# Kernel tuning notes

Hardware: AMD Instinct MI355X
Metric: run time of the kernel (lower is better)

Reference implementation:

```python
import jax, jax.numpy as jnp
import numpy as np

C = 512
IC = C // 2
BN_EPS = 1e-5

def conv1x1(x, w, b):
    # x: (b,c,h,w), w: (o,c), b: (o,)
    return jnp.einsum('bchw,oc->bohw', x, w) + b[None, :, None, None]

def setup_inputs() -> dict:
    key = jax.random.key(0)
    ks = jax.random.split(key, 9)
    b, h, w = 8, 48, 48
    x = jax.random.normal(ks[0], (b, C, h, w), dtype=jnp.float32)
    s = 1.0 / np.sqrt(C)
    g_w = jax.random.normal(ks[1], (IC, C), dtype=jnp.float32) * s
    g_b = jnp.zeros((IC,), jnp.float32)
    theta_w = jax.random.normal(ks[2], (IC, C), dtype=jnp.float32) * s
    theta_b = jnp.zeros((IC,), jnp.float32)
    phi_w = jax.random.normal(ks[3], (IC, C), dtype=jnp.float32) * s
    phi_b = jnp.zeros((IC,), jnp.float32)
    w_w = jax.random.normal(ks[4], (C, IC), dtype=jnp.float32) * (1.0 / np.sqrt(IC))
    w_b = jnp.zeros((C,), jnp.float32)
    # BatchNorm affine params: initialized to 0 per nn.init.constant_ in source
    bn_gamma = jnp.zeros((C,), jnp.float32)
    bn_beta = jnp.zeros((C,), jnp.float32)
    return {"x": x, "g_w": g_w, "g_b": g_b, "theta_w": theta_w, "theta_b": theta_b,
            "phi_w": phi_w, "phi_b": phi_b, "w_w": w_w, "w_b": w_b,
            "bn_gamma": bn_gamma, "bn_beta": bn_beta}

def reference(x, g_w, g_b, theta_w, theta_b, phi_w, phi_b, w_w, w_b, bn_gamma, bn_beta):
    b, c, h, w = x.shape
    hw = h * w
    g_x = conv1x1(x, g_w, g_b).reshape(b, IC, hw).transpose(0, 2, 1)      # (b,hw,ic)
    theta_x = conv1x1(x, theta_w, theta_b).reshape(b, IC, hw).transpose(0, 2, 1)  # (b,hw,ic)
    phi_x = conv1x1(x, phi_w, phi_b).reshape(b, IC, hw)                    # (b,ic,hw)
    f = jnp.einsum('bqc,bck->bqk', theta_x, phi_x)                         # (b,hw,hw), unscaled
    f_div_C = jax.nn.softmax(f, axis=-1)
    y = jnp.einsum('bqk,bkc->bqc', f_div_C, g_x)                           # (b,hw,ic)
    y = y.transpose(0, 2, 1).reshape(b, IC, h, w)
    wy = conv1x1(y, w_w, w_b)                                              # (b,c,h,w)
    # BatchNorm2d in training mode: batch statistics over (b,h,w)
    mean = jnp.mean(wy, axis=(0, 2, 3), keepdims=True)
    var = jnp.var(wy, axis=(0, 2, 3), keepdims=True)
    wy_bn = (wy - mean) / jnp.sqrt(var + BN_EPS)
    wy_bn = wy_bn * bn_gamma[None, :, None, None] + bn_beta[None, :, None, None]
    return wy_bn + x
```

## Files before the change

kernel.cpp:

```cpp
#include <hip/hip_runtime.h>
#include <hip/hip_bf16.h>
#include <stdint.h>

constexpr int Bn  = 8;
constexpr int Cc  = 512;
constexpr int ICc = 256;
constexpr int HWc = 48 * 48;
constexpr float BN_EPS = 1e-5f;

typedef unsigned short u16;
typedef __attribute__((ext_vector_type(8))) short short8;
typedef __attribute__((ext_vector_type(4))) float f32x4;

__device__ __forceinline__ u16 f2bf(float f) {
    uint32_t u = __builtin_bit_cast(uint32_t, f);
    u += 0x7fffu + ((u >> 16) & 1u);
    return (u16)(u >> 16);
}
__device__ __forceinline__ float bf2f(u16 h) {
    uint32_t u = ((uint32_t)h) << 16;
    return __builtin_bit_cast(float, u);
}
__device__ __forceinline__ void load_lds16(const void* g, void* l) {
    __builtin_amdgcn_global_load_lds(
        (const __attribute__((address_space(1))) void*)(uintptr_t)g,
        (__attribute__((address_space(3))) void*)(uintptr_t)l, 16, 0, 0);
}
template <int N> __device__ __forceinline__ void wait_vmcnt() {
    if constexpr (N == 0)      asm volatile("s_waitcnt vmcnt(0)" ::: "memory");
    else if constexpr (N == 3) asm volatile("s_waitcnt vmcnt(3)" ::: "memory");
    else if constexpr (N == 4) asm volatile("s_waitcnt vmcnt(4)" ::: "memory");
    else if constexpr (N == 6) asm volatile("s_waitcnt vmcnt(6)" ::: "memory");
    else if constexpr (N == 8) asm volatile("s_waitcnt vmcnt(8)" ::: "memory");
}
__device__ __forceinline__ void wait_lgkm0() {
    asm volatile("s_waitcnt lgkmcnt(0)" ::: "memory");
}
__device__ __forceinline__ void barrier_fenced() {
    __builtin_amdgcn_s_barrier();
    asm volatile("" ::: "memory");
}

__global__ __launch_bounds__(256)
void cast_front(const float* __restrict__ th_w, const float* __restrict__ ph_w,
                const float* __restrict__ g_w, const float* __restrict__ th_b,
                const float* __restrict__ ph_b, u16* __restrict__ wcat,
                float* __restrict__ bias_thph) {
    int idx = blockIdx.x * 256 + threadIdx.x;
    if (idx < 98304) {
        const float4* src;
        if (idx < 32768)       src = (const float4*)th_w + idx;
        else if (idx < 65536)  src = (const float4*)ph_w + (idx - 32768);
        else                   src = (const float4*)g_w  + (idx - 65536);
        float4 v = *src;
        ushort4 o;
        o.x = f2bf(v.x); o.y = f2bf(v.y); o.z = f2bf(v.z); o.w = f2bf(v.w);
        ((ushort4*)wcat)[idx] = o;
    } else if (idx < 98816) {
        int i = idx - 98304;
        bias_thph[i] = (i < 256) ? th_b[i] : ph_b[i - 256];
    }
}

__global__ __launch_bounds__(256)
void cast_w(const float* __restrict__ a, u16* __restrict__ out) {
    int idx = blockIdx.x * 256 + threadIdx.x;
    float4 v = ((const float4*)a)[idx];
    ushort4 o;
    o.x = f2bf(v.x); o.y = f2bf(v.y); o.z = f2bf(v.z); o.w = f2bf(v.w);
    ((ushort4*)out)[idx] = o;
}

__global__ __launch_bounds__(256)
void transpose_cast_x(const float* __restrict__ x, u16* __restrict__ xt) {
    __shared__ float t[64][33];
    const int b = blockIdx.z;
    const int p0 = blockIdx.x * 32;
    const int c0 = blockIdx.y * 64;
    const int tx = threadIdx.x & 31, ty = threadIdx.x >> 5;
    const float* xb = x + (size_t)b * Cc * HWc;
#pragma unroll
    for (int r = 0; r < 8; ++r)
        t[r * 8 + ty][tx] = xb[(size_t)(c0 + r * 8 + ty) * HWc + p0 + tx];
    __syncthreads();
    u16* xtb = xt + (size_t)b * HWc * Cc;
    const int cc = (threadIdx.x & 31) * 2, pp = threadIdx.x >> 5;
#pragma unroll
    for (int r = 0; r < 4; ++r) {
        int p = r * 8 + pp;
        ushort2 v;
        v.x = f2bf(t[cc][p]);
        v.y = f2bf(t[cc + 1][p]);
        *(ushort2*)&xtb[(size_t)(p0 + p) * Cc + c0 + cc] = v;
    }
}

template <int TM, int STORE, bool STATS>
__global__ __launch_bounds__(256, 2)
void mfma_gemm(const u16* __restrict__ A, const u16* __restrict__ B,
               void* __restrict__ Cout, const float* __restrict__ bias,
               int bias_mode, int K, int ldA, int ldB, int ldC,
               size_t sA, size_t sB, size_t sC,
               float* __restrict__ s0g, float* __restrict__ s1g) {
    constexpr int MI  = TM / 32;
    constexpr int LPS = (TM == 128) ? 4 : 3;
    __shared__ __align__(16) u16 As[3][TM * 32];
    __shared__ __align__(16) u16 Bs[3][128 * 32];
    const int bz = blockIdx.z;
    const int m0 = blockIdx.y * TM, n0 = blockIdx.x * 128;
    const u16* Ab = A + (size_t)bz * sA + (size_t)m0 * ldA;
    const u16* Bb = B + (size_t)bz * sB + (size_t)n0 * ldB;
    const int tid = threadIdx.x, lane = tid & 63, w = tid >> 6;
    const int wm = (w & 1) * (TM / 2);
    const int wn = (w >> 1) * 64;
    const int quad = lane >> 4, m16 = lane & 15;

    f32x4 acc[MI][4];
#pragma unroll
    for (int i = 0; i < MI; ++i)
#pragma unroll
        for (int j = 0; j < 4; ++j) acc[i][j] = (f32x4){0.f, 0.f, 0.f, 0.f};

    const int L0 = 2 * w * 64 + lane, L1 = L0 + 64;
    const int br0 = L0 >> 2, bc0 = ((L0 & 3) ^ ((L0 >> 3) & 3)) * 8;
    const int br1 = L1 >> 2, bc1 = ((L1 & 3) ^ ((L1 >> 3) & 3)) * 8;
    const int ar0 = (TM == 128) ? br0 : (tid >> 2);
    const int ac0 = (TM == 128) ? bc0 : (((tid & 3) ^ ((tid >> 3) & 3)) * 8);

    auto stage = [&](int buf, int k0) {
        if (TM == 128) {
            load_lds16(Ab + (size_t)ar0 * ldA + k0 + ac0, &As[buf][2 * w * 512]);
            load_lds16(Ab + (size_t)br1 * ldA + k0 + bc1, &As[buf][(2 * w + 1) * 512]);
        } else {
            load_lds16(Ab + (size_t)ar0 * ldA + k0 + ac0, &As[buf][w * 512]);
        }
        load_lds16(Bb + (size_t)br0 * ldB + k0 + bc0, &Bs[buf][2 * w * 512]);
        load_lds16(Bb + (size_t)br1 * ldB + k0 + bc1, &Bs[buf][(2 * w + 1) * 512]);
    };

    const int sq = (quad ^ ((m16 >> 1) & 3)) * 8;

    auto compute = [&](int buf) {
        short8 af[MI], bfv[4];
#pragma unroll
        for (int i = 0; i < MI; ++i)
            af[i] = *(const short8*)&As[buf][(wm + i * 16 + m16) * 32 + sq];
#pragma unroll
        for (int j = 0; j < 4; ++j)
            bfv[j] = *(const short8*)&Bs[buf][(wn + j * 16 + m16) * 32 + sq];
#pragma unroll
        for (int i = 0; i < MI; ++i)
#pragma unroll
            for (int j = 0; j < 4; ++j)
                acc[i][j] = __builtin_amdgcn_mfma_f32_16x16x32_bf16(
                    af[i], bfv[j], acc[i][j], 0, 0, 0);
    };

    const int nt = K / 32;
    stage(0, 0);
    stage(1, 32);

    int cur = 0;
    for (int t = 0; t < nt - 2; ++t) {
        int nxt = cur + 2; if (nxt >= 3) nxt -= 3;
        stage(nxt, (t + 2) * 32);
        wait_vmcnt<2 * LPS>();
        barrier_fenced();
        compute(cur);
        wait_lgkm0();
        barrier_fenced();
        ++cur; if (cur == 3) cur = 0;
    }
    wait_vmcnt<LPS>();
    barrier_fenced();
    compute(cur);
    wait_lgkm0();
    barrier_fenced();
    ++cur; if (cur == 3) cur = 0;
    wait_vmcnt<0>();
    barrier_fenced();
    compute(cur);

    if (bias_mode) {
#pragma unroll
        for (int i = 0; i < MI; ++i)
#pragma unroll
            for (int j = 0; j < 4; ++j)
#pragma unroll
                for (int r = 0; r < 4; ++r)
                    acc[i][j][r] += (bias_mode == 2)
                        ? bias[m0 + wm + i * 16 + quad * 4 + r]
                        : bias[n0 + wn + j * 16 + m16];
    }

    if (STORE == 0) {
        u16* C = (u16*)Cout + (size_t)bz * sC;
#pragma unroll
        for (int i = 0; i < MI; ++i) {
            int m = m0 + wm + i * 16 + quad * 4;
#pragma unroll
            for (int j = 0; j < 4; ++j) {
                int n = n0 + wn + j * 16 + m16;
#pragma unroll
                for (int r = 0; r < 4; ++r)
                    C[(size_t)(m + r) * ldC + n] = f2bf(acc[i][j][r]);
            }
        }
    } else {
        float* C = (float*)Cout + (size_t)bz * sC;
#pragma unroll
        for (int i = 0; i < MI; ++i) {
            int m = m0 + wm + i * 16 + quad * 4;
#pragma unroll
            for (int j = 0; j < 4; ++j) {
                int n = n0 + wn + j * 16 + m16;
#pragma unroll
                for (int r = 0; r < 4; ++r)
                    C[(size_t)(m + r) * ldC + n] = acc[i][j][r];
            }
        }
    }

    if (STATS) {
#pragma unroll
        for (int i = 0; i < MI; ++i) {
#pragma unroll
            for (int r = 0; r < 4; ++r) {
                float v0 = 0.f, v1 = 0.f;
#pragma unroll
                for (int j = 0; j < 4; ++j) {
                    float v = acc[i][j][r];
                    v0 += v;
                    v1 = fmaf(v, v, v1);
                }
#pragma unroll
                for (int off = 8; off; off >>= 1) {
                    v0 += __shfl_down(v0, off, 16);
                    v1 += __shfl_down(v1, off, 16);
                }
                if (m16 == 0) {
                    int m = m0 + wm + i * 16 + quad * 4 + r;
                    atomicAdd(&s0g[m], v0);
                    atomicAdd(&s1g[m], v1);
                }
            }
        }
    }
}

__global__ __launch_bounds__(192)
void softmax_rows(u16* __restrict__ S) {
    const int b = blockIdx.x & 7;
    const int q = blockIdx.x >> 3;
    u16* row = S + ((size_t)b * HWc + q) * (size_t)HWc;
    const int tid = threadIdx.x;

    float v[12];
#pragma unroll
    for (int c = 0; c < 3; ++c) {
        uint2 raw = *(const uint2*)&row[(c * 192 + tid) * 4];
        v[c * 4 + 0] = bf2f((u16)(raw.x & 0xffff));
        v[c * 4 + 1] = bf2f((u16)(raw.x >> 16));
        v[c * 4 + 2] = bf2f((u16)(raw.y & 0xffff));
        v[c * 4 + 3] = bf2f((u16)(raw.y >> 16));
    }
    float m = v[0];
#pragma unroll
    for (int i = 1; i < 12; ++i) m = fmaxf(m, v[i]);
#pragma unroll
    for (int off = 32; off; off >>= 1) m = fmaxf(m, __shfl_down(m, off, 64));
    __shared__ float redm[3], reds[3];
    if ((tid & 63) == 0) redm[tid >> 6] = m;
    __syncthreads();
    m = fmaxf(fmaxf(redm[0], redm[1]), redm[2]);

    float s = 0.f;
#pragma unroll
    for (int i = 0; i < 12; ++i) { v[i] = __expf(v[i] - m); s += v[i]; }
#pragma unroll
    for (int off = 32; off; off >>= 1) s += __shfl_down(s, off, 64);
    if ((tid & 63) == 0) reds[tid >> 6] = s;
    __syncthreads();
    const float rinv = 1.0f / (reds[0] + reds[1] + reds[2]);

#pragma unroll
    for (int c = 0; c < 3; ++c) {
        uint2 o;
        o.x = (uint32_t)f2bf(v[c * 4 + 0] * rinv) |
              ((uint32_t)f2bf(v[c * 4 + 1] * rinv) << 16);
        o.y = (uint32_t)f2bf(v[c * 4 + 2] * rinv) |
              ((uint32_t)f2bf(v[c * 4 + 3] * rinv) << 16);
        *(uint2*)&row[(c * 192 + tid) * 4] = o;
    }
}

__global__ __launch_bounds__(256)
void bn_apply(const float* __restrict__ wy, const float* __restrict__ x,
              const float* __restrict__ s0, const float* __restrict__ s1,
              const float* __restrict__ gamma, const float* __restrict__ beta,
              float* __restrict__ out) {
    const size_t i4 = (size_t)blockIdx.x * 256 + threadIdx.x;
    const size_t base = i4 * 4;
    const int o = (int)((base / HWc) % Cc);
    const float N = (float)(Bn * HWc);
    const float mean = s0[o] / N;
    const float var  = s1[o] / N - mean * mean;
    const float rstd = rsqrtf(var + BN_EPS);
    const float ga = gamma[o];
    const float be = beta[o];
    const float4 w4 = ((const float4*)wy)[i4];
    const float4 x4 = ((const float4*)x)[i4];
    float4 r;
    r.x = (w4.x - mean) * rstd * ga + be + x4.x;
    r.y = (w4.y - mean) * rstd * ga + be + x4.y;
    r.z = (w4.z - mean) * rstd * ga + be + x4.z;
    r.w = (w4.w - mean) * rstd * ga + be + x4.w;
    ((float4*)out)[i4] = r;
}

extern "C" void kernel_launch(void* const* d_in, const int* in_sizes, int n_in,
                              void* d_out, int out_size, void* d_ws, size_t ws_size,
                              hipStream_t stream) {
    const float* x     = (const float*)d_in[0];
    const float* g_w   = (const float*)d_in[1];
    const float* g_b   = (const float*)d_in[2];
    const float* th_w  = (const float*)d_in[3];
    const float* th_b  = (const float*)d_in[4];
    const float* ph_w  = (const float*)d_in[5];
    const float* ph_b  = (const float*)d_in[6];
    const float* w_w   = (const float*)d_in[7];
    const float* w_b   = (const float*)d_in[8];
    const float* gamma = (const float*)d_in[9];
    const float* beta  = (const float*)d_in[10];

    char* base = (char*)d_ws;
    const size_t SZT = (size_t)Bn * HWc * ICc * 2;
    u16* thph = (u16*)base;
    u16* g    = (u16*)(base + 2 * SZT);
    char* Sreg = base + 3 * SZT;
    u16* S    = (u16*)Sreg;
    u16* xt   = (u16*)Sreg;
    u16* wcat = (u16*)(Sreg + (size_t)Bn * HWc * Cc * 2);
    float* bias_thph = (float*)(Sreg + (size_t)Bn * HWc * Cc * 2 + 786432);
    u16* y    = (u16*)base;
    u16* wbf2 = (u16*)(base + SZT);
    float* stats = (float*)(base + SZT + 262144);
    float* wy = (float*)Sreg;

    dim3 blk(256);
    const u16* thphw = wcat;
    const u16* gwb   = wcat + 262144;

    cast_front<<<dim3(386), blk, 0, stream>>>(th_w, ph_w, g_w, th_b, ph_b,
                                              wcat, bias_thph);
    transpose_cast_x<<<dim3(HWc / 32, Cc / 64, Bn), blk, 0, stream>>>(x, xt);

    mfma_gemm<128, 0, false><<<dim3(4, 18, Bn), blk, 0, stream>>>(
        xt, thphw, thph, bias_thph, 1, Cc, Cc, Cc, 512,
        (size_t)HWc * Cc, 0, (size_t)HWc * 512, nullptr, nullptr);

    mfma_gemm<64, 0, false><<<dim3(18, 4, Bn), blk, 0, stream>>>(
        gwb, xt, g, g_b, 2, Cc, Cc, Cc, HWc,
        0, (size_t)HWc * Cc, (size_t)ICc * HWc, nullptr, nullptr);

    mfma_gemm<128, 0, false><<<dim3(18, 18, Bn), blk, 0, stream>>>(
        thph, thph + 256, S, nullptr, 0, ICc, 512, 512, HWc,
        (size_t)HWc * 512, (size_t)HWc * 512, (size_t)HWc * HWc,
        nullptr, nullptr);

    cast_w<<<dim3(128), blk, 0, stream>>>(w_w, wbf2);
    hipMemsetAsync(stats, 0, 2 * Cc * sizeof(float), stream);

    softmax_rows<<<dim3(Bn * HWc), dim3(192), 0, stream>>>(S);

    mfma_gemm<64, 0, false><<<dim3(2, 36, Bn), blk, 0, stream>>>(
        S, g, y, nullptr, 0, HWc, HWc, HWc, ICc,
        (size_t)HWc * HWc, (size_t)ICc * HWc, (size_t)HWc * ICc,
        nullptr, nullptr);

    mfma_gemm<128, 1, true><<<dim3(18, 4, Bn), blk, 0, stream>>>(
        wbf2, y, wy, w_b, 2, ICc, ICc, ICc, HWc,
        0, (size_t)HWc * ICc, (size_t)Cc * HWc, stats, stats + Cc);

    bn_apply<<<dim3((Bn * Cc * HWc) / 4 / 256), blk, 0, stream>>>(
        wy, x, stats, stats + Cc, gamma, beta, (float*)d_out);
}
```

Baseline: 321.1 us.

## Fuse QK^T, softmax and PV into a single flash-attention kernel

Replaces the separate S=QK^T GEMM, row softmax and PV GEMM with one online-softmax kernel that keeps 64-key tiles of scores in LDS and accumulates the output with running max/sum rescaling. This removes the write and re-read of the full bf16 score matrix (8×2304×2304) and two kernel launches, and the workspace layout is rearranged accordingly. In exchange only 288 blocks are launched, V is read straight from global memory without LDS staging, and there are several barriers per tile, which may limit occupancy and latency hiding.

```diff
diff --git a/kernel.cpp b/kernel.cpp
--- a/kernel.cpp
+++ b/kernel.cpp
@@ -248,49 +248,187 @@
     }
 }
 
-__global__ __launch_bounds__(192)
-void softmax_rows(u16* __restrict__ S) {
-    const int b = blockIdx.x & 7;
-    const int q = blockIdx.x >> 3;
-    u16* row = S + ((size_t)b * HWc + q) * (size_t)HWc;
-    const int tid = threadIdx.x;
-
-    float v[12];
-#pragma unroll
-    for (int c = 0; c < 3; ++c) {
-        uint2 raw = *(const uint2*)&row[(c * 192 + tid) * 4];
-        v[c * 4 + 0] = bf2f((u16)(raw.x & 0xffff));
-        v[c * 4 + 1] = bf2f((u16)(raw.x >> 16));
-        v[c * 4 + 2] = bf2f((u16)(raw.y & 0xffff));
-        v[c * 4 + 3] = bf2f((u16)(raw.y >> 16));
-    }
-    float m = v[0];
-#pragma unroll
-    for (int i = 1; i < 12; ++i) m = fmaxf(m, v[i]);
-#pragma unroll
-    for (int off = 32; off; off >>= 1) m = fmaxf(m, __shfl_down(m, off, 64));
-    __shared__ float redm[3], reds[3];
-    if ((tid & 63) == 0) redm[tid >> 6] = m;
+__global__ __launch_bounds__(256, 2)
+void fused_attn(const u16* __restrict__ thph, const u16* __restrict__ gmat,
+                u16* __restrict__ y) {
+    __shared__ __align__(16) u16 Ks[2][64 * 256];
+    __shared__ __align__(16) u16 Sl[64 * 68];
+    __shared__ float alpha_lds[64];
+
+    const int id = blockIdx.x;
+    const int b = id & 7, qi = id >> 3;
+    const int q0 = qi * 64;
+    const u16* tB = thph + (size_t)b * HWc * 512;
+    const u16* gB = gmat + (size_t)b * ICc * HWc;
+    const int tid = threadIdx.x, lane = tid & 63, w = tid >> 6;
+    const int quad = lane >> 4, m16 = lane & 15;
+    const int wq = (w & 1) * 32, wk = (w >> 1) * 32;
+    const int wv = w * 64;
+
+    short8 qf[2][8];
+#pragma unroll
+    for (int i = 0; i < 2; ++i)
+#pragma unroll
+        for (int ds = 0; ds < 8; ++ds)
+            qf[i][ds] = *(const short8*)&tB[(size_t)(q0 + wq + i * 16 + m16) * 512
+                                            + ds * 32 + quad * 8];
+
+    auto stageK = [&](int buf, int k0) {
+#pragma unroll
+        for (int u = 0; u < 8; ++u) {
+            int s = (w * 8 + u) * 64 + lane;
+            int r = s >> 5;
+            int c = s & 31;
+            int sc = c ^ (r & 7);
+            load_lds16(tB + (size_t)(k0 + r) * 512 + 256 + sc * 8,
+                       &Ks[buf][(w * 8 + u) * 512]);
+        }
+    };
+
+    const int sr = w * 16 + (lane >> 2);
+    const int scol = (lane & 3) * 16;
+    float mrow = -3.0e38f, lrow = 0.f;
+
+    f32x4 acc2[4][4];
+#pragma unroll
+    for (int i = 0; i < 4; ++i)
+#pragma unroll
+        for (int j = 0; j < 4; ++j) acc2[i][j] = (f32x4){0.f, 0.f, 0.f, 0.f};
+
+    stageK(0, 0);
+
+    for (int t = 0; t < 36; ++t) {
+        const int buf = t & 1;
+        if (t + 1 < 36) {
+            stageK(buf ^ 1, (t + 1) * 64);
+            wait_vmcnt<8>();
+        } else {
+            wait_vmcnt<0>();
+        }
+        barrier_fenced();
+
+        f32x4 acc1[2][2];
+#pragma unroll
+        for (int i = 0; i < 2; ++i)
+#pragma unroll
+            for (int j = 0; j < 2; ++j) acc1[i][j] = (f32x4){0.f, 0.f, 0.f, 0.f};
+        const u16* kb = &Ks[buf][0];
+#pragma unroll
+        for (int ds = 0; ds < 8; ++ds) {
+            short8 kf[2];
+#pragma unroll
+            for (int j = 0; j < 2; ++j) {
+                int kr = wk + j * 16 + m16;
+                int c  = (ds * 4 + quad) ^ (m16 & 7);
+                kf[j] = *(const short8*)&kb[kr * 256 + c * 8];
+            }
+#pragma unroll
+            for (int i = 0; i < 2; ++i)
+#pragma unroll
+                for (int j = 0; j < 2; ++j)
+                    acc1[i][j] = __builtin_amdgcn_mfma_f32_16x16x32_bf16(
+                        qf[i][ds], kf[j], acc1[i][j], 0, 0, 0);
+        }
+
+#pragma unroll
+        for (int i = 0; i < 2; ++i)
+#pragma unroll
+            for (int j = 0; j < 2; ++j)
+#pragma unroll
+                for (int r = 0; r < 4; ++r)
+                    Sl[(wq + i * 16 + quad * 4 + r) * 68 + wk + j * 16 + m16] =
+                        f2bf(acc1[i][j][r]);
+        wait_lgkm0();
+        barrier_fenced();
+
+        {
+            u16* srow = &Sl[sr * 68 + scol];
+            float v[16];
+            short4 r0 = *(const short4*)&srow[0];
+            short4 r1 = *(const short4*)&srow[4];
+            short4 r2 = *(const short4*)&srow[8];
+            short4 r3 = *(const short4*)&srow[12];
+            v[0]=bf2f((u16)r0.x); v[1]=bf2f((u16)r0.y); v[2]=bf2f((u16)r0.z); v[3]=bf2f((u16)r0.w);
+            v[4]=bf2f((u16)r1.x); v[5]=bf2f((u16)r1.y); v[6]=bf2f((u16)r1.z); v[7]=bf2f((u16)r1.w);
+            v[8]=bf2f((u16)r2.x); v[9]=bf2f((u16)r2.y); v[10]=bf2f((u16)r2.z); v[11]=bf2f((u16)r2.w);
+            v[12]=bf2f((u16)r3.x); v[13]=bf2f((u16)r3.y); v[14]=bf2f((u16)r3.z); v[15]=bf2f((u16)r3.w);
+            float tm = v[0];
+#pragma unroll
+            for (int k = 1; k < 16; ++k) tm = fmaxf(tm, v[k]);
+            tm = fmaxf(tm, __shfl_xor(tm, 1, 64));
+            tm = fmaxf(tm, __shfl_xor(tm, 2, 64));
+            float mn = fmaxf(mrow, tm);
+            float a  = __expf(mrow - mn);
+            float rs = 0.f;
+#pragma unroll
+            for (int k = 0; k < 16; ++k) { v[k] = __expf(v[k] - mn); rs += v[k]; }
+            rs += __shfl_xor(rs, 1, 64);
+            rs += __shfl_xor(rs, 2, 64);
+            lrow = lrow * a + rs;
+            mrow = mn;
+            ushort4 o0 = {f2bf(v[0]), f2bf(v[1]), f2bf(v[2]), f2bf(v[3])};
+            ushort4 o1 = {f2bf(v[4]), f2bf(v[5]), f2bf(v[6]), f2bf(v[7])};
+            ushort4 o2 = {f2bf(v[8]), f2bf(v[9]), f2bf(v[10]), f2bf(v[11])};
+            ushort4 o3 = {f2bf(v[12]), f2bf(v[13]), f2bf(v[14]), f2bf(v[15])};
+            *(ushort4*)&srow[0]  = o0;
+            *(ushort4*)&srow[4]  = o1;
+            *(ushort4*)&srow[8]  = o2;
+            *(ushort4*)&srow[12] = o3;
+            if ((lane & 3) == 0) alpha_lds[sr] = a;
+        }
+        wait_lgkm0();
+        barrier_fenced();
+
+        f32x4 al[4];
+#pragma unroll
+        for (int i = 0; i < 4; ++i)
+            al[i] = *(const f32x4*)&alpha_lds[i * 16 + quad * 4];
+#pragma unroll
+        for (int i = 0; i < 4; ++i)
+#pragma unroll
+            for (int j2 = 0; j2 < 4; ++j2)
+#pragma unroll
+                for (int r = 0; r < 4; ++r) acc2[i][j2][r] *= al[i][r];
+
+        const int kbase = t * 64;
+#pragma unroll
+        for (int ks = 0; ks < 2; ++ks) {
+            short8 pa[4];
+#pragma unroll
+            for (int i = 0; i < 4; ++i) {
+                const u16* pr = &Sl[(i * 16 + m16) * 68 + ks * 32 + quad * 8];
+                short4 lo = *(const short4*)&pr[0];
+                short4 hi = *(const short4*)&pr[4];
+                pa[i] = (short8){lo.x, lo.y, lo.z, lo.w, hi.x, hi.y, hi.z, hi.w};
+            }
+            short8 vb[4];
+#pragma unroll
+            for (int j2 = 0; j2 < 4; ++j2)
+                vb[j2] = *(const short8*)&gB[(size_t)(wv + j2 * 16 + m16) * HWc
+                                             + kbase + ks * 32 + quad * 8];
+#pragma unroll
+            for (int i = 0; i < 4; ++i)
+#pragma unroll
+                for (int j2 = 0; j2 < 4; ++j2)
+                    acc2[i][j2] = __builtin_amdgcn_mfma_f32_16x16x32_bf16(
+                        pa[i], vb[j2], acc2[i][j2], 0, 0, 0);
+        }
+    }
+
     __syncthreads();
-    m = fmaxf(fmaxf(redm[0], redm[1]), redm[2]);
-
-    float s = 0.f;
-#pragma unroll
-    for (int i = 0; i < 12; ++i) { v[i] = __expf(v[i] - m); s += v[i]; }
-#pragma unroll
-    for (int off = 32; off; off >>= 1) s += __shfl_down(s, off, 64);
-    if ((tid & 63) == 0) reds[tid >> 6] = s;
+    if ((lane & 3) == 0) alpha_lds[sr] = 1.0f / lrow;
     __syncthreads();
-    const float rinv = 1.0f / (reds[0] + reds[1] + reds[2]);
-
-#pragma unroll
-    for (int c = 0; c < 3; ++c) {
-        uint2 o;
-        o.x = (uint32_t)f2bf(v[c * 4 + 0] * rinv) |
-              ((uint32_t)f2bf(v[c * 4 + 1] * rinv) << 16);
-        o.y = (uint32_t)f2bf(v[c * 4 + 2] * rinv) |
-              ((uint32_t)f2bf(v[c * 4 + 3] * rinv) << 16);
-        *(uint2*)&row[(c * 192 + tid) * 4] = o;
+
+    u16* yB = y + (size_t)b * HWc * ICc;
+#pragma unroll
+    for (int i = 0; i < 4; ++i) {
+        f32x4 li = *(const f32x4*)&alpha_lds[i * 16 + quad * 4];
+#pragma unroll
+        for (int j2 = 0; j2 < 4; ++j2)
+#pragma unroll
+            for (int r = 0; r < 4; ++r)
+                yB[(size_t)(q0 + i * 16 + quad * 4 + r) * ICc + wv + j2 * 16 + m16] =
+                    f2bf(acc2[i][j2][r] * li[r]);
     }
 }
 
@@ -338,14 +476,13 @@
     u16* thph = (u16*)base;
     u16* g    = (u16*)(base + 2 * SZT);
     char* Sreg = base + 3 * SZT;
-    u16* S    = (u16*)Sreg;
     u16* xt   = (u16*)Sreg;
     u16* wcat = (u16*)(Sreg + (size_t)Bn * HWc * Cc * 2);
     float* bias_thph = (float*)(Sreg + (size_t)Bn * HWc * Cc * 2 + 786432);
-    u16* y    = (u16*)base;
-    u16* wbf2 = (u16*)(base + SZT);
-    float* stats = (float*)(base + SZT + 262144);
-    float* wy = (float*)Sreg;
+    u16* y    = (u16*)Sreg;
+    float* wy = (float*)(Sreg + SZT);
+    u16* wbf2 = (u16*)(Sreg + SZT + (size_t)Bn * Cc * HWc * 4);
+    float* stats = (float*)(Sreg + SZT + (size_t)Bn * Cc * HWc * 4 + 262144);
 
     dim3 blk(256);
     const u16* thphw = wcat;
@@ -363,20 +500,10 @@
         gwb, xt, g, g_b, 2, Cc, Cc, Cc, HWc,
         0, (size_t)HWc * Cc, (size_t)ICc * HWc, nullptr, nullptr);
 
-    mfma_gemm<128, 0, false><<<dim3(18, 18, Bn), blk, 0, stream>>>(
-        thph, thph + 256, S, nullptr, 0, ICc, 512, 512, HWc,
-        (size_t)HWc * 512, (size_t)HWc * 512, (size_t)HWc * HWc,
-        nullptr, nullptr);
-
     cast_w<<<dim3(128), blk, 0, stream>>>(w_w, wbf2);
     hipMemsetAsync(stats, 0, 2 * Cc * sizeof(float), stream);
 
-    softmax_rows<<<dim3(Bn * HWc), dim3(192), 0, stream>>>(S);
-
-    mfma_gemm<64, 0, false><<<dim3(2, 36, Bn), blk, 0, stream>>>(
-        S, g, y, nullptr, 0, HWc, HWc, HWc, ICc,
-        (size_t)HWc * HWc, (size_t)ICc * HWc, (size_t)HWc * ICc,
-        nullptr, nullptr);
+    fused_attn<<<dim3(288), blk, 0, stream>>>(thph, g, y);
 
     mfma_gemm<128, 1, true><<<dim3(18, 4, Bn), blk, 0, stream>>>(
         wbf2, y, wy, w_b, 2, ICc, ICc, ICc, HWc,
```

Result: no change. 323.1 us (+0.6%).

## Fuse QK^T, softmax and PV into a flash-attention style kernel

Applied to the files above, without the earlier changes.

Replaces the separate score GEMM, row softmax and probability-times-V GEMM with one fused kernel that uses online softmax over key tiles of 32, so the full HW×HW score matrix is never written to or read from global memory. K and V tiles are double-buffered in LDS through direct global-to-LDS loads, and both products use 32x32x16 bf16 MFMA. Workspace offsets are rearranged because the S buffer is gone. The cost is a small grid of 576 blocks of 128 threads and heavy per-block register use, which may limit occupancy.

```diff
diff --git a/kernel.cpp b/kernel.cpp
--- a/kernel.cpp
+++ b/kernel.cpp
@@ -11,6 +11,8 @@
 typedef unsigned short u16;
 typedef __attribute__((ext_vector_type(8))) short short8;
 typedef __attribute__((ext_vector_type(4))) float f32x4;
+typedef __attribute__((ext_vector_type(16))) float f32x16;
+typedef __attribute__((ext_vector_type(4))) unsigned int u32x4;
 
 __device__ __forceinline__ u16 f2bf(float f) {
     uint32_t u = __builtin_bit_cast(uint32_t, f);
@@ -248,50 +250,130 @@
     }
 }
 
-__global__ __launch_bounds__(192)
-void softmax_rows(u16* __restrict__ S) {
-    const int b = blockIdx.x & 7;
-    const int q = blockIdx.x >> 3;
-    u16* row = S + ((size_t)b * HWc + q) * (size_t)HWc;
-    const int tid = threadIdx.x;
-
-    float v[12];
-#pragma unroll
-    for (int c = 0; c < 3; ++c) {
-        uint2 raw = *(const uint2*)&row[(c * 192 + tid) * 4];
-        v[c * 4 + 0] = bf2f((u16)(raw.x & 0xffff));
-        v[c * 4 + 1] = bf2f((u16)(raw.x >> 16));
-        v[c * 4 + 2] = bf2f((u16)(raw.y & 0xffff));
-        v[c * 4 + 3] = bf2f((u16)(raw.y >> 16));
-    }
-    float m = v[0];
-#pragma unroll
-    for (int i = 1; i < 12; ++i) m = fmaxf(m, v[i]);
-#pragma unroll
-    for (int off = 32; off; off >>= 1) m = fmaxf(m, __shfl_down(m, off, 64));
-    __shared__ float redm[3], reds[3];
-    if ((tid & 63) == 0) redm[tid >> 6] = m;
-    __syncthreads();
-    m = fmaxf(fmaxf(redm[0], redm[1]), redm[2]);
-
-    float s = 0.f;
-#pragma unroll
-    for (int i = 0; i < 12; ++i) { v[i] = __expf(v[i] - m); s += v[i]; }
-#pragma unroll
-    for (int off = 32; off; off >>= 1) s += __shfl_down(s, off, 64);
-    if ((tid & 63) == 0) reds[tid >> 6] = s;
-    __syncthreads();
-    const float rinv = 1.0f / (reds[0] + reds[1] + reds[2]);
-
-#pragma unroll
-    for (int c = 0; c < 3; ++c) {
-        uint2 o;
-        o.x = (uint32_t)f2bf(v[c * 4 + 0] * rinv) |
-              ((uint32_t)f2bf(v[c * 4 + 1] * rinv) << 16);
-        o.y = (uint32_t)f2bf(v[c * 4 + 2] * rinv) |
-              ((uint32_t)f2bf(v[c * 4 + 3] * rinv) << 16);
-        *(uint2*)&row[(c * 192 + tid) * 4] = o;
-    }
+__global__ __launch_bounds__(128, 2)
+void fused_attn(const u16* __restrict__ thph, const u16* __restrict__ gmat,
+                u16* __restrict__ y) {
+    __shared__ __align__(16) u16 Ks[2][8192];
+    __shared__ __align__(16) u16 Vs[2][8192];
+    const int id = blockIdx.x;
+    const int b = id & 7, qt = id >> 3;
+    const int q0 = qt * 32;
+    const u16* tB = thph + (size_t)b * HWc * 512;
+    const u16* gB = gmat + (size_t)b * ICc * HWc;
+    const int tid = threadIdx.x, lane = tid & 63, w = tid >> 6;
+    const int l31 = lane & 31, h = lane >> 5;
+
+    short8 qf[16];
+#pragma unroll
+    for (int ds = 0; ds < 16; ++ds)
+        qf[ds] = *(const short8*)&tB[(size_t)(q0 + l31) * 512 + ds * 16 + h * 8];
+
+    auto stage = [&](int buf, int t) {
+        const int k0 = t * 32;
+#pragma unroll
+        for (int u = 0; u < 8; ++u) {
+            const int su = w * 8 + u;
+            load_lds16(tB + (size_t)(k0 + l31) * 512 + 256 + (su * 2 + h) * 8,
+                       &Ks[buf][su * 512]);
+        }
+#pragma unroll
+        for (int u = 0; u < 8; ++u) {
+            const int su = w * 8 + u;
+            load_lds16(gB + (size_t)((su & 3) * 64 + lane) * HWc + k0 + (su >> 2) * 8,
+                       &Vs[buf][su * 512]);
+        }
+    };
+
+    float mrow = -3.0e38f, lrow = 0.f;
+    f32x16 acc2[4];
+#pragma unroll
+    for (int vt = 0; vt < 4; ++vt)
+#pragma unroll
+        for (int e = 0; e < 16; ++e) acc2[vt][e] = 0.f;
+
+    stage(0, 0);
+    wait_vmcnt<0>();
+    barrier_fenced();
+
+    constexpr int NT = 72;
+    for (int t = 0; t < NT; ++t) {
+        const int buf = t & 1;
+        if (t + 1 < NT) stage(buf ^ 1, t + 1);
+
+        f32x16 acc1;
+#pragma unroll
+        for (int e = 0; e < 16; ++e) acc1[e] = 0.f;
+#pragma unroll
+        for (int ds = 0; ds < 16; ++ds) {
+            short8 kf = *(const short8*)&Ks[buf][((ds * 2 + h) * 32 + l31) * 8];
+            acc1 = __builtin_amdgcn_mfma_f32_32x32x16_bf16(kf, qf[ds], acc1, 0, 0, 0);
+        }
+
+        float tm = acc1[0];
+#pragma unroll
+        for (int e = 1; e < 16; ++e) tm = fmaxf(tm, acc1[e]);
+        tm = fmaxf(tm, __shfl_xor(tm, 32, 64));
+        const float mn = fmaxf(mrow, tm);
+        const float al = __expf(mrow - mn);
+        float rs = 0.f;
+#pragma unroll
+        for (int e = 0; e < 16; ++e) { acc1[e] = __expf(acc1[e] - mn); rs += acc1[e]; }
+        rs += __shfl_xor(rs, 32, 64);
+        lrow = lrow * al + rs;
+        mrow = mn;
+
+        uint32_t olo[4], ohi[4], slo[4], shi[4];
+#pragma unroll
+        for (int g = 0; g < 4; ++g) {
+            olo[g] = (uint32_t)f2bf(acc1[4 * g + 0]) |
+                     ((uint32_t)f2bf(acc1[4 * g + 1]) << 16);
+            ohi[g] = (uint32_t)f2bf(acc1[4 * g + 2]) |
+                     ((uint32_t)f2bf(acc1[4 * g + 3]) << 16);
+            slo[g] = (uint32_t)__shfl_xor((int)olo[g], 32, 64);
+            shi[g] = (uint32_t)__shfl_xor((int)ohi[g], 32, 64);
+        }
+
+#pragma unroll
+        for (int vt = 0; vt < 4; ++vt)
+#pragma unroll
+            for (int e = 0; e < 16; ++e) acc2[vt][e] *= al;
+
+#pragma unroll
+        for (int ks = 0; ks < 2; ++ks) {
+            const uint32_t f0 = h ? slo[2 * ks + 1] : olo[2 * ks];
+            const uint32_t f1 = h ? shi[2 * ks + 1] : ohi[2 * ks];
+            const uint32_t f2 = h ? olo[2 * ks + 1] : slo[2 * ks];
+            const uint32_t f3 = h ? ohi[2 * ks + 1] : shi[2 * ks];
+            const u32x4 pw = (u32x4){f0, f1, f2, f3};
+            const short8 pf = __builtin_bit_cast(short8, pw);
+#pragma unroll
+            for (int vt = 0; vt < 4; ++vt) {
+                short8 vf = *(const short8*)
+                    &Vs[buf][((ks * 2 + h) * 256 + w * 128 + vt * 32 + l31) * 8];
+                acc2[vt] = __builtin_amdgcn_mfma_f32_32x32x16_bf16(
+                    vf, pf, acc2[vt], 0, 0, 0);
+            }
+        }
+
+        if (t + 1 < NT) {
+            wait_vmcnt<0>();
+            barrier_fenced();
+        }
+    }
+
+    const float linv = 1.0f / lrow;
+    u16* yB = y + (size_t)b * HWc * ICc + (size_t)(q0 + l31) * ICc + w * 128;
+#pragma unroll
+    for (int vt = 0; vt < 4; ++vt)
+#pragma unroll
+        for (int g = 0; g < 4; ++g) {
+            ushort4 o;
+            o.x = f2bf(acc2[vt][4 * g + 0] * linv);
+            o.y = f2bf(acc2[vt][4 * g + 1] * linv);
+            o.z = f2bf(acc2[vt][4 * g + 2] * linv);
+            o.w = f2bf(acc2[vt][4 * g + 3] * linv);
+            *(ushort4*)&yB[vt * 32 + g * 8 + h * 4] = o;
+        }
 }
 
 __global__ __launch_bounds__(256)
@@ -338,14 +420,13 @@
     u16* thph = (u16*)base;
     u16* g    = (u16*)(base + 2 * SZT);
     char* Sreg = base + 3 * SZT;
-    u16* S    = (u16*)Sreg;
     u16* xt   = (u16*)Sreg;
     u16* wcat = (u16*)(Sreg + (size_t)Bn * HWc * Cc * 2);
     float* bias_thph = (float*)(Sreg + (size_t)Bn * HWc * Cc * 2 + 786432);
-    u16* y    = (u16*)base;
-    u16* wbf2 = (u16*)(base + SZT);
-    float* stats = (float*)(base + SZT + 262144);
-    float* wy = (float*)Sreg;
+    u16* y    = (u16*)Sreg;
+    float* wy = (float*)(Sreg + SZT);
+    u16* wbf2 = (u16*)(Sreg + SZT + (size_t)Bn * Cc * HWc * 4);
+    float* stats = (float*)(Sreg + SZT + (size_t)Bn * Cc * HWc * 4 + 262144);
 
     dim3 blk(256);
     const u16* thphw = wcat;
@@ -363,20 +444,10 @@
         gwb, xt, g, g_b, 2, Cc, Cc, Cc, HWc,
         0, (size_t)HWc * Cc, (size_t)ICc * HWc, nullptr, nullptr);
 
-    mfma_gemm<128, 0, false><<<dim3(18, 18, Bn), blk, 0, stream>>>(
-        thph, thph + 256, S, nullptr, 0, ICc, 512, 512, HWc,
-        (size_t)HWc * 512, (size_t)HWc * 512, (size_t)HWc * HWc,
-        nullptr, nullptr);
-
     cast_w<<<dim3(128), blk, 0, stream>>>(w_w, wbf2);
     hipMemsetAsync(stats, 0, 2 * Cc * sizeof(float), stream);
 
-    softmax_rows<<<dim3(Bn * HWc), dim3(192), 0, stream>>>(S);
-
-    mfma_gemm<64, 0, false><<<dim3(2, 36, Bn), blk, 0, stream>>>(
-        S, g, y, nullptr, 0, HWc, HWc, HWc, ICc,
-        (size_t)HWc * HWc, (size_t)ICc * HWc, (size_t)HWc * ICc,
-        nullptr, nullptr);
+    fused_attn<<<dim3(576), dim3(128), 0, stream>>>(thph, g, y);
 
     mfma_gemm<128, 1, true><<<dim3(18, 4, Bn), blk, 0, stream>>>(
         wbf2, y, wy, w_b, 2, ICc, ICc, ICc, HWc,
```

After: 453.3 us. +41.1%, slower.
